# Optimization experiments

Hardware: AMD Instinct MI355X
Metric: run time of the kernel (lower is better)

Reference implementation:

```python
import jax, jax.numpy as jnp
import numpy as np

B, NX, NY = 4, 128, 128
DIM, DH, HEADS, LATENT, DOUT = 128, 64, 8, 64, 128
KM = 3
KD = DH * KM          # per-head low-rank-kernel dim (192)
SCALING = 1.0         # kernel_multiplier<=4 and softmax=False -> scaling_factor
ROT_SCALE = 64.0      # 1/min_freq of continuous RotaryEmbedding (min_freq=1/64)
EPS = 1e-5


def layer_norm(x, g, b):
    m = x.mean(-1, keepdims=True)
    v = jnp.var(x, axis=-1, keepdims=True)
    return (x - m) * jax.lax.rsqrt(v + EPS) * g + b


def pooling_reducer(x, Win, g, b, W1, b1, W2, b2):
    # x: [b, n, m, c] -> mean over axis 2 -> PreNorm(MLP with gated GELU) -> [b, n, latent]
    h = (x @ Win).mean(axis=2)
    h = layer_norm(h, g, b)
    h = h @ W1 + b1
    c = h.shape[-1] // 2
    h = jax.nn.gelu(h[..., :c], approximate=False) * h[..., c:]
    return h @ W2 + b2


def rotary(t, pos):
    # t: [b,h,n,d], pos: [n] continuous coordinates
    d = t.shape[-1]
    inv_freq = 1.0 / (10000.0 ** (jnp.arange(0, d, 2, dtype=jnp.float32) / d))
    f = (pos * ROT_SCALE)[:, None] * inv_freq          # [n, d//2]
    f = jnp.concatenate([f, f], axis=-1)               # [n, d]
    cos, sin = jnp.cos(f), jnp.sin(f)
    x1, x2 = jnp.split(t, 2, axis=-1)
    rot = jnp.concatenate([-x2, x1], axis=-1)          # rotate_half (half-split variant)
    return t * cos + rot * sin


def low_rank_kernel(u, pos, Wqk):
    # u: [b, n, latent] -> kernel K: [b, h, n, n]
    b, n, _ = u.shape
    qk = u @ Wqk                                       # [b, n, 2*h*KD]
    q, k = jnp.split(qk, 2, axis=-1)
    q = q.reshape(b, n, HEADS, KD).transpose(0, 2, 1, 3)
    k = k.reshape(b, n, HEADS, KD).transpose(0, 2, 1, 3)
    q = rotary(q, pos)
    k = rotary(k, pos)
    return jnp.einsum('bhid,bhjd->bhij', q, k) * SCALING


def setup_inputs():
    key = jax.random.key(0)
    ks = jax.random.split(key, 16)
    s = 0.02
    def rn(k, shape):
        return jax.random.normal(k, shape, dtype=jnp.float32) * s
    return {
        'u': jax.random.normal(ks[0], (B, NX, NY, DIM), dtype=jnp.float32),
        'pos_x': jnp.sort(jax.random.uniform(ks[1], (NX,), dtype=jnp.float32)),
        'pos_y': jnp.sort(jax.random.uniform(ks[2], (NY,), dtype=jnp.float32)),
        'ln_g': jnp.ones((DIM,), jnp.float32),
        'ln_b': jnp.zeros((DIM,), jnp.float32),
        'Wv': rn(ks[3], (DIM, HEADS * DH)),
        'Win': rn(ks[4], (DIM, DIM)),
        'px_Win': rn(ks[5], (DIM, DIM)),
        'px_g': jnp.ones((DIM,), jnp.float32),
        'px_b': jnp.zeros((DIM,), jnp.float32),
        'px_W1': rn(ks[6], (DIM, 2 * DIM)),
        'px_b1': jnp.zeros((2 * DIM,), jnp.float32),
        'px_W2': rn(ks[7], (DIM, LATENT)),
        'px_b2': jnp.zeros((LATENT,), jnp.float32),
        'py_Win': rn(ks[8], (DIM, DIM)),
        'py_g': jnp.ones((DIM,), jnp.float32),
        'py_b': jnp.zeros((DIM,), jnp.float32),
        'py_W1': rn(ks[9], (DIM, 2 * DIM)),
        'py_b1': jnp.zeros((2 * DIM,), jnp.float32),
        'py_W2': rn(ks[10], (DIM, LATENT)),
        'py_b2': jnp.zeros((LATENT,), jnp.float32),
        'Wqk_x': rn(ks[11], (LATENT, 2 * HEADS * KD)),
        'Wqk_y': rn(ks[12], (LATENT, 2 * HEADS * KD)),
        'Wo1': rn(ks[13], (HEADS * DH, DOUT)),
        'Wo2': rn(ks[14], (DOUT, DOUT)),
    }


def reference(u, pos_x, pos_y, ln_g, ln_b, Wv, Win,
              px_Win, px_g, px_b, px_W1, px_b1, px_W2, px_b2,
              py_Win, py_g, py_b, py_W1, py_b1, py_W2, py_b2,
              Wqk_x, Wqk_y, Wo1, Wo2):
    un = layer_norm(u, ln_g, ln_b)                      # [b,nx,ny,dim]
    v = un @ Wv                                         # [b,nx,ny,h*dh]
    ui = un @ Win
    ux = pooling_reducer(ui, px_Win, px_g, px_b, px_W1, px_b1, px_W2, px_b2)                       # [b,nx,L]
    uy = pooling_reducer(ui.transpose(0, 2, 1, 3), py_Win, py_g, py_b, py_W1, py_b1, py_W2, py_b2)  # [b,ny,L]
    kx = low_rank_kernel(ux, pos_x, Wqk_x)              # [b,h,nx,nx]
    ky = low_rank_kernel(uy, pos_y, Wqk_y)              # [b,h,ny,ny]
    b, nx, ny, _ = u.shape
    vphi = v.reshape(b, nx, ny, HEADS, DH).transpose(0, 3, 1, 2, 4)   # b h i l c
    t = jnp.einsum('bhij,bhjmc->bhimc', kx, vphi)       # attend along x axis
    t = jnp.einsum('bhlm,bhimc->bhilc', ky, t)          # attend along y axis
    t = t.transpose(0, 2, 3, 1, 4).reshape(b, nx, ny, HEADS * DH)
    # InstanceNorm2d applied to a channels-LAST tensor (as in the original repo):
    # torch treats dim1 (nx) as channels, normalizing over (ny, h*dh) per (b, nx), no affine.
    m = t.mean(axis=(2, 3), keepdims=True)
    var = t.var(axis=(2, 3), keepdims=True)
    t = (t - m) * jax.lax.rsqrt(var + EPS)
    h = jax.nn.gelu(t @ Wo1, approximate=False)
    return h @ Wo2
```

## Files before the change

kernel.cpp:

```cpp
#include <hip/hip_runtime.h>
#include <math.h>

#define ROWS 65536
#define KDD 192

typedef __attribute__((ext_vector_type(8))) short bfrag;
typedef __attribute__((ext_vector_type(4))) float facc;

__device__ inline unsigned short bf16r(float x) {
  union { float f; unsigned u; } v; v.f = x;
  unsigned r = v.u + 0x7fffu + ((v.u >> 16) & 1u);
  return (unsigned short)(r >> 16);
}
__device__ inline float bf2f(unsigned short h) {
  union { unsigned u; float f; } v; v.u = ((unsigned)h) << 16; return v.f;
}
__device__ inline float gelu_f(float x) {
  return x * 0.5f * (1.f + erff(x * 0.70710678f));
}
__device__ __forceinline__ void gload16(const void* g, void* l) {
  __builtin_amdgcn_global_load_lds((const __attribute__((address_space(1))) unsigned int*)g,
                                   (__attribute__((address_space(3))) unsigned int*)l,
                                   16, 0, 0);
}

__global__ __launch_bounds__(256) void k_ln(const float* __restrict__ x,
                                            const float* __restrict__ g,
                                            const float* __restrict__ bb,
                                            unsigned short* __restrict__ y) {
  int t = threadIdx.x;
  int w = t >> 6, lane = t & 63;
  size_t row = (size_t)blockIdx.x * 4 + w;
  float2 v = *(const float2*)(x + row * 128 + lane * 2);
  float s = v.x + v.y, s2 = v.x * v.x + v.y * v.y;
#pragma unroll
  for (int off = 1; off < 64; off <<= 1) {
    s += __shfl_xor(s, off, 64);
    s2 += __shfl_xor(s2, off, 64);
  }
  float mean = s * (1.f / 128.f);
  float var = s2 * (1.f / 128.f) - mean * mean;
  float r = rsqrtf(var + 1e-5f);
  float2 gg = *(const float2*)(g + lane * 2);
  float2 bv = *(const float2*)(bb + lane * 2);
  unsigned h0 = bf16r((v.x - mean) * r * gg.x + bv.x);
  unsigned h1 = bf16r((v.y - mean) * r * gg.y + bv.y);
  *(unsigned*)(y + row * 128 + lane * 2) = h0 | (h1 << 16);
}

__global__ __launch_bounds__(128) void k_means(const unsigned short* __restrict__ un,
                                               float* __restrict__ mx, float* __restrict__ my) {
  int blk = blockIdx.x;
  int c = threadIdx.x;
  if (blk < 512) {
    const unsigned short* p = un + (size_t)blk * 16384 + c;
    float s = 0;
    for (int j = 0; j < 128; j++) s += bf2f(p[(size_t)j * 128]);
    mx[(size_t)blk * 128 + c] = s * (1.f / 128.f);
  } else {
    int bj = blk - 512;
    int b = bj >> 7, j = bj & 127;
    const unsigned short* p = un + (size_t)b * 2097152 + (size_t)j * 128 + c;
    float s = 0;
    for (int i = 0; i < 128; i++) s += bf2f(p[(size_t)i * 16384]);
    my[(size_t)bj * 128 + c] = s * (1.f / 128.f);
  }
}

__global__ __launch_bounds__(256) void k_wprep(const float* __restrict__ Wv,
                                               const float* __restrict__ Wo1,
                                               const float* __restrict__ Wo2,
                                               unsigned short* __restrict__ WvT,
                                               unsigned short* __restrict__ Wo1T,
                                               unsigned short* __restrict__ Wo2T,
                                               float* __restrict__ scol) {
  int blk = blockIdx.x, t = threadIdx.x;
  if (blk < 256) {
    int idx = blk * 256 + t;
    int c = idx >> 7, r = idx & 127;
    WvT[(size_t)c * 128 + r] = bf16r(Wv[(size_t)r * 512 + c]);
  } else if (blk < 512) {
    int idx = (blk - 256) * 256 + t;
    int n = idx >> 9, k = idx & 511;
    Wo1T[(size_t)n * 512 + k] = bf16r(Wo1[(size_t)k * 128 + n]);
  } else if (blk < 576) {
    int idx = (blk - 512) * 256 + t;
    int n = idx >> 7, k = idx & 127;
    Wo2T[n * 128 + k] = bf16r(Wo2[k * 128 + n]);
  } else {
    if (t < 128) {
      float a = 0;
      for (int k = 0; k < 512; k++) a += bf2f(bf16r(Wo1[k * 128 + t]));
      scol[t] = a;
    }
  }
}

__global__ __launch_bounds__(256) void k_gemmz(const float* __restrict__ A0,
                                               const float* __restrict__ B0,
                                               float* __restrict__ C0,
                                               const float* __restrict__ A1,
                                               const float* __restrict__ B1,
                                               float* __restrict__ C1,
                                               int K, int lda, int ldb, int ldc) {
  const float* A = blockIdx.z ? A1 : A0;
  const float* Bm = blockIdx.z ? B1 : B0;
  float* C = blockIdx.z ? C1 : C0;
  __shared__ float As[16][64];
  __shared__ float Bs[16][64];
  int tid = threadIdx.x;
  int n0 = blockIdx.x * 64, m0 = blockIdx.y * 64;
  int tx = tid & 15, ty = tid >> 4;
  float acc[4][4] = {};
  int la_m = tid >> 2, la_k = (tid & 3) * 4;
  int lb_k = tid >> 4, lb_n = (tid & 15) * 4;
  for (int k0 = 0; k0 < K; k0 += 16) {
    float4 a4 = *(const float4*)(A + (size_t)(m0 + la_m) * lda + k0 + la_k);
    As[la_k + 0][la_m] = a4.x; As[la_k + 1][la_m] = a4.y;
    As[la_k + 2][la_m] = a4.z; As[la_k + 3][la_m] = a4.w;
    float4 b4 = *(const float4*)(Bm + (size_t)(k0 + lb_k) * ldb + n0 + lb_n);
    *(float4*)&Bs[lb_k][lb_n] = b4;
    __syncthreads();
#pragma unroll
    for (int kk = 0; kk < 16; kk++) {
      float4 av = *(const float4*)&As[kk][ty * 4];
      float4 bv = *(const float4*)&Bs[kk][tx * 4];
      float a[4] = {av.x, av.y, av.z, av.w};
      float b[4] = {bv.x, bv.y, bv.z, bv.w};
#pragma unroll
      for (int i = 0; i < 4; i++)
#pragma unroll
        for (int j = 0; j < 4; j++) acc[i][j] += a[i] * b[j];
    }
    __syncthreads();
  }
#pragma unroll
  for (int i = 0; i < 4; i++) {
    float4 o;
    o.x = acc[i][0]; o.y = acc[i][1]; o.z = acc[i][2]; o.w = acc[i][3];
    *(float4*)(C + (size_t)(m0 + ty * 4 + i) * ldc + n0 + tx * 4) = o;
  }
}

__global__ __launch_bounds__(128) void k_pool2(const float* __restrict__ in0, const float* __restrict__ in1,
                                               const float* __restrict__ Wc0, const float* __restrict__ Wc1,
                                               const float* __restrict__ g0, const float* __restrict__ g1,
                                               const float* __restrict__ bb0, const float* __restrict__ bb1,
                                               const float* __restrict__ W10, const float* __restrict__ W11,
                                               const float* __restrict__ b10, const float* __restrict__ b11,
                                               const float* __restrict__ W20, const float* __restrict__ W21,
                                               const float* __restrict__ b20, const float* __restrict__ b21,
                                               float* __restrict__ o0, float* __restrict__ o1) {
  int sel = blockIdx.y;
  const float* in = sel ? in1 : in0;  const float* Wc = sel ? Wc1 : Wc0;
  const float* g = sel ? g1 : g0;     const float* bb = sel ? bb1 : bb0;
  const float* W1 = sel ? W11 : W10;  const float* b1 = sel ? b11 : b10;
  const float* W2 = sel ? W21 : W20;  const float* b2 = sel ? b21 : b20;
  float* out = sel ? o1 : o0;
  int row = blockIdx.x;
  int t = threadIdx.x;
  __shared__ float xin[128], h1[128], h3[128];
  __shared__ float ps[2], ps2[2];
  xin[t] = in[(size_t)row * 128 + t];
  __syncthreads();
  float a = 0;
  for (int k = 0; k < 128; k++) a += xin[k] * Wc[k * 128 + t];
  float s = a, s2 = a * a;
  for (int off = 32; off > 0; off >>= 1) {
    s += __shfl_down(s, off, 64);
    s2 += __shfl_down(s2, off, 64);
  }
  if ((t & 63) == 0) { ps[t >> 6] = s; ps2[t >> 6] = s2; }
  __syncthreads();
  float S = ps[0] + ps[1], S2 = ps2[0] + ps2[1];
  float mean = S * (1.f / 128.f);
  float var = S2 * (1.f / 128.f) - mean * mean;
  float r = rsqrtf(var + 1e-5f);
  h1[t] = (a - mean) * r * g[t] + bb[t];
  __syncthreads();
  float u1 = b1[t], u2 = b1[t + 128];
  for (int k = 0; k < 128; k++) {
    float hv = h1[k];
    u1 += hv * W1[k * 256 + t];
    u2 += hv * W1[k * 256 + t + 128];
  }
  h3[t] = gelu_f(u1) * u2;
  __syncthreads();
  if (t < 64) {
    float o = b2[t];
    for (int k = 0; k < 128; k++) o += h3[k] * W2[k * 64 + t];
    out[(size_t)row * 64 + t] = o;
  }
}

__global__ __launch_bounds__(192) void k_rot2(const float* __restrict__ qk0, const float* __restrict__ qk1,
                                              const float* __restrict__ pos0, const float* __restrict__ pos1,
                                              float* __restrict__ qr0, float* __restrict__ qr1,
                                              float* __restrict__ kr0, float* __restrict__ kr1) {
  int sel = blockIdx.y;
  const float* qk = sel ? qk1 : qk0;
  const float* pos = sel ? pos1 : pos0;
  float* qr = sel ? qr1 : qr0;
  float* kr = sel ? kr1 : kr0;
  int bn = blockIdx.x;
  int b = bn >> 7, n = bn & 127;
  int d = threadIdx.x;
  int fi = d % 96;
  float inv = expf(-logf(10000.f) * ((float)fi / 96.f));
  float f = pos[n] * 64.f * inv;
  float cs = cosf(f), sn = sinf(f);
  int partner = d < 96 ? d + 96 : d - 96;
  float sgn = d < 96 ? -1.f : 1.f;
  for (int h = 0; h < 8; h++) {
    float q = qk[(size_t)bn * 3072 + h * 192 + d];
    float qp = qk[(size_t)bn * 3072 + h * 192 + partner];
    float kx = qk[(size_t)bn * 3072 + 1536 + h * 192 + d];
    float kp = qk[(size_t)bn * 3072 + 1536 + h * 192 + partner];
    size_t o = ((size_t)(b * 8 + h) * 128 + n) * 192 + d;
    qr[o] = q * cs + sgn * qp * sn;
    kr[o] = kx * cs + sgn * kp * sn;
  }
}

__global__ __launch_bounds__(512) void k_qkt2(const float* __restrict__ Q0, const float* __restrict__ K0,
                                              unsigned short* __restrict__ C0,
                                              const float* __restrict__ Q1, const float* __restrict__ K1,
                                              unsigned short* __restrict__ C1) {
  int z = blockIdx.z;
  int bh = z & 31;
  const float* Qb = (z < 32 ? Q0 : Q1) + (size_t)bh * 128 * KDD;
  const float* Kb = (z < 32 ? K0 : K1) + (size_t)bh * 128 * KDD;
  unsigned short* Cb = (z < 32 ? C0 : C1) + (size_t)bh * 128 * 128;
  __shared__ float As[16][64];
  __shared__ float Bs[16][64];
  int tid = threadIdx.x;
  int i0 = blockIdx.y * 64, j0 = blockIdx.x * 64;
  int tx = tid & 15, ty = tid >> 4;
  float acc[2][4] = {};
  int l_m = tid >> 3, l_k = (tid & 7) * 2;
  for (int k0 = 0; k0 < KDD; k0 += 16) {
    float2 a2 = *(const float2*)(Qb + (size_t)(i0 + l_m) * KDD + k0 + l_k);
    As[l_k + 0][l_m] = a2.x; As[l_k + 1][l_m] = a2.y;
    float2 b2 = *(const float2*)(Kb + (size_t)(j0 + l_m) * KDD + k0 + l_k);
    Bs[l_k + 0][l_m] = b2.x; Bs[l_k + 1][l_m] = b2.y;
    __syncthreads();
#pragma unroll
    for (int kk = 0; kk < 16; kk++) {
      float2 av = *(const float2*)&As[kk][ty * 2];
      float4 bv = *(const float4*)&Bs[kk][tx * 4];
      float a[2] = {av.x, av.y};
      float b[4] = {bv.x, bv.y, bv.z, bv.w};
#pragma unroll
      for (int i = 0; i < 2; i++)
#pragma unroll
        for (int j = 0; j < 4; j++) acc[i][j] += a[i] * b[j];
    }
    __syncthreads();
  }
#pragma unroll
  for (int i = 0; i < 2; i++) {
    unsigned h0 = bf16r(acc[i][0]), h1 = bf16r(acc[i][1]);
    unsigned h2 = bf16r(acc[i][2]), h3 = bf16r(acc[i][3]);
    uint2 pk;
    pk.x = h0 | (h1 << 16);
    pk.y = h2 | (h3 << 16);
    *(uint2*)(Cb + (size_t)(i0 + ty * 2 + i) * 128 + j0 + tx * 4) = pk;
  }
}


__global__ __launch_bounds__(256) void k_vt(const unsigned short* __restrict__ WvT,
                                            const unsigned short* __restrict__ un,
                                            unsigned short* __restrict__ vT) {
  int nt = blockIdx.x;
  __shared__ __align__(16) unsigned short Bs[16384];
  int tid = threadIdx.x;
  int w = tid >> 6, lane = tid & 63, quad = lane >> 4, l16 = lane & 15;
  int wr = w >> 1, wc = w & 1;
  {
    const unsigned short* sbp = un + (size_t)nt * 16384;
#pragma unroll
    for (int q = 0; q < 8; q++) {
      int rbase = w * 32 + q * 4;
      int r = rbase + quad;
      gload16(sbp + (size_t)r * 128 + ((l16 ^ (r & 15)) << 3), &Bs[rbase * 128]);
    }
  }
  __syncthreads();
  facc zf = {0.f, 0.f, 0.f, 0.f};
#pragma unroll
  for (int mt = 0; mt < 4; mt++) {
    const unsigned short* ap = WvT + (size_t)mt * 128 * 128;
    facc acc[4][4];
#pragma unroll
    for (int lt = 0; lt < 4; lt++)
#pragma unroll
      for (int xt = 0; xt < 4; xt++) acc[lt][xt] = zf;
#pragma unroll
    for (int k0 = 0; k0 < 4; k0++) {
      int chunk = ((k0 * 4 + quad) ^ l16) << 3;
      bfrag bv[4], av[4];
#pragma unroll
      for (int lt = 0; lt < 4; lt++)
        bv[lt] = *(const bfrag*)&Bs[((wc * 4 + lt) * 16 + l16) * 128 + chunk];
#pragma unroll
      for (int xt = 0; xt < 4; xt++)
        av[xt] = *(const bfrag*)(ap + (size_t)((wr * 4 + xt) * 16 + l16) * 128 + k0 * 32 + quad * 8);
      __builtin_amdgcn_s_setprio(1);
#pragma unroll
      for (int lt = 0; lt < 4; lt++)
#pragma unroll
        for (int xt = 0; xt < 4; xt++)
          acc[lt][xt] = __builtin_amdgcn_mfma_f32_16x16x32_bf16(bv[lt], av[xt], acc[lt][xt], 0, 0, 0);
      __builtin_amdgcn_s_setprio(0);
    }
#pragma unroll
    for (int xt = 0; xt < 4; xt++) {
      int hc = mt * 128 + (wr * 4 + xt) * 16 + l16;
      unsigned short* dst = vT + (size_t)hc * 65536 + nt * 128 + quad * 4;
#pragma unroll
      for (int lt = 0; lt < 4; lt++) {
        facc a = acc[lt][xt];
        uint2 p;
        p.x = (unsigned)bf16r(a[0]) | ((unsigned)bf16r(a[1]) << 16);
        p.y = (unsigned)bf16r(a[2]) | ((unsigned)bf16r(a[3]) << 16);
        *(uint2*)(dst + (wc * 4 + lt) * 16) = p;
      }
    }
  }
}

__global__ __launch_bounds__(256, 2) void k_fuse12(const unsigned short* __restrict__ kxall,
                                                   const unsigned short* __restrict__ kyall,
                                                   const unsigned short* __restrict__ vT,
                                                   unsigned short* __restrict__ ttp,
                                                   float* __restrict__ sb,
                                                   float* __restrict__ s2b) {
  int blk = blockIdx.x;
  int bh = blk >> 4, strip = blk & 15;
  int b = bh >> 3, h = bh & 7;
  __shared__ __align__(16) unsigned short Ky[16384];
  __shared__ __align__(16) unsigned short Vs[16384];
  int tid = threadIdx.x;
  int w = tid >> 6, lane = tid & 63, quad = lane >> 4, l16 = lane & 15;
  int wr = w >> 1, wc = w & 1;

  {
    const unsigned short* kb = kyall + (size_t)bh * 16384;
#pragma unroll
    for (int q = 0; q < 8; q++) {
      int rbase = w * 32 + q * 4;
      int r = rbase + quad;
      gload16(kb + (size_t)r * 128 + ((l16 ^ (r & 15)) << 3), &Ky[rbase * 128]);
    }
  }
  bfrag axf[4][4];
  {
    const unsigned short* xb = kxall + (size_t)bh * 16384;
#pragma unroll
    for (int it = 0; it < 4; it++) {
      int i = (wr * 4 + it) * 16 + l16;
#pragma unroll
      for (int k0 = 0; k0 < 4; k0++)
        axf[it][k0] = *(const bfrag*)(xb + (size_t)i * 128 + k0 * 32 + quad * 8);
    }
  }

  float s[4] = {0.f, 0.f, 0.f, 0.f}, s2[4] = {0.f, 0.f, 0.f, 0.f};
  facc zf = {0.f, 0.f, 0.f, 0.f};

  for (int cc = 0; cc < 4; cc++) {
    int c = strip * 4 + cc;
    if (cc) __syncthreads();
    {
      const unsigned short* vb = vT + (size_t)(h * 64 + c) * 65536 + (size_t)b * 16384;
#pragma unroll
      for (int q = 0; q < 8; q++) {
        int rbase = w * 32 + q * 4;
        int r = rbase + quad;
        gload16(vb + (size_t)r * 128 + ((l16 ^ (r & 15)) << 3), &Vs[rbase * 128]);
      }
    }
    __syncthreads();

    facc a1[4][4];
#pragma unroll
    for (int xt = 0; xt < 4; xt++)
#pragma unroll
      for (int lt = 0; lt < 4; lt++) a1[xt][lt] = zf;
#pragma unroll
    for (int k0 = 0; k0 < 4; k0++) {
      int chunk = ((k0 * 4 + quad) ^ l16) << 3;
      bfrag av[4], bv[4];
#pragma unroll
      for (int xt = 0; xt < 4; xt++)
        av[xt] = *(const bfrag*)&Vs[((wr * 4 + xt) * 16 + l16) * 128 + chunk];
#pragma unroll
      for (int lt = 0; lt < 4; lt++)
        bv[lt] = *(const bfrag*)&Ky[((wc * 4 + lt) * 16 + l16) * 128 + chunk];
      __builtin_amdgcn_s_setprio(1);
#pragma unroll
      for (int xt = 0; xt < 4; xt++)
#pragma unroll
        for (int lt = 0; lt < 4; lt++)
          a1[xt][lt] = __builtin_amdgcn_mfma_f32_16x16x32_bf16(av[xt], bv[lt], a1[xt][lt], 0, 0, 0);
      __builtin_amdgcn_s_setprio(0);
    }
    __syncthreads();
#pragma unroll
    for (int xt = 0; xt < 4; xt++) {
      int xc = (wr * 4 + xt) * 2 + (quad >> 1);
      int xo = (quad & 1) * 4;
#pragma unroll
      for (int lt = 0; lt < 4; lt++) {
        int l = (wc * 4 + lt) * 16 + l16;
        unsigned p0 = (unsigned)bf16r(a1[xt][lt][0]) | ((unsigned)bf16r(a1[xt][lt][1]) << 16);
        unsigned p1 = (unsigned)bf16r(a1[xt][lt][2]) | ((unsigned)bf16r(a1[xt][lt][3]) << 16);
        uint2 p; p.x = p0; p.y = p1;
        *(uint2*)&Vs[l * 128 + ((xc ^ (l & 15)) << 3) + xo] = p;
      }
    }
    __syncthreads();

    facc a2[4][4];
#pragma unroll
    for (int st = 0; st < 4; st++)
#pragma unroll
      for (int it = 0; it < 4; it++) a2[st][it] = zf;
#pragma unroll
    for (int k0 = 0; k0 < 4; k0++) {
      int chunk = ((k0 * 4 + quad) ^ l16) << 3;
      bfrag sv[4];
#pragma unroll
      for (int st = 0; st < 4; st++)
        sv[st] = *(const bfrag*)&Vs[((wc * 4 + st) * 16 + l16) * 128 + chunk];
      __builtin_amdgcn_s_setprio(1);
#pragma unroll
      for (int st = 0; st < 4; st++)
#pragma unroll
        for (int it = 0; it < 4; it++)
          a2[st][it] = __builtin_amdgcn_mfma_f32_16x16x32_bf16(sv[st], axf[it][k0], a2[st][it], 0, 0, 0);
      __builtin_amdgcn_s_setprio(0);
    }
    {
      unsigned short* dst = ttp + ((size_t)(bh * 64 + c) << 14);
#pragma unroll
      for (int st = 0; st < 4; st++) {
        int l0 = (wc * 4 + st) * 16 + quad * 4;
#pragma unroll
        for (int it = 0; it < 4; it++) {
          int i = (wr * 4 + it) * 16 + l16;
          float f0 = a2[st][it][0], f1 = a2[st][it][1];
          float f2 = a2[st][it][2], f3 = a2[st][it][3];
          unsigned p0 = (unsigned)bf16r(f0) | ((unsigned)bf16r(f1) << 16);
          unsigned p1 = (unsigned)bf16r(f2) | ((unsigned)bf16r(f3) << 16);
          uint2 p; p.x = p0; p.y = p1;
          *(uint2*)(dst + (size_t)i * 128 + l0) = p;
          s[it] += (f0 + f1) + (f2 + f3);
          s2[it] += f0 * f0 + f1 * f1 + f2 * f2 + f3 * f3;
        }
      }
    }
  }
#pragma unroll
  for (int it = 0; it < 4; it++) {
    float v = s[it], v2 = s2[it];
    v += __shfl_xor(v, 16, 64);  v += __shfl_xor(v, 32, 64);
    v2 += __shfl_xor(v2, 16, 64); v2 += __shfl_xor(v2, 32, 64);
    if (quad == 0) {
      int i = (wr * 4 + it) * 16 + l16;
      atomicAdd(&sb[b * 128 + i], v);
      atomicAdd(&s2b[b * 128 + i], v2);
    }
  }
}

__global__ __launch_bounds__(256) void k_tail2(const unsigned short* __restrict__ ttp,
                                               const unsigned short* __restrict__ Wo1T,
                                               const unsigned short* __restrict__ Wo2T,
                                               float* __restrict__ out,
                                               const float* __restrict__ sb,
                                               const float* __restrict__ s2b,
                                               const float* __restrict__ sc) {
  int blk = blockIdx.x;
  int b = blk >> 7, i = blk & 127;
  __shared__ __align__(16) unsigned short As[16384];
  __shared__ __align__(16) unsigned short Bs[16384];
  int tid = threadIdx.x;
  int w = tid >> 6, lane = tid & 63, quad = lane >> 4, l16 = lane & 15;
  facc zf = {0.f, 0.f, 0.f, 0.f};
  facc a1[2][8];
#pragma unroll
  for (int a = 0; a < 2; a++)
#pragma unroll
    for (int bq = 0; bq < 8; bq++) a1[a][bq] = zf;
  for (int kc = 0; kc < 4; kc++) {
    if (kc) __syncthreads();
    {
      int r = tid >> 1, half = tid & 1;
      int hc = kc * 128 + r;
      const unsigned short* src = ttp + (((size_t)(b * 8 + (hc >> 6)) * 64 + (hc & 63)) * 128 + i) * 128 + half * 64;
#pragma unroll
      for (int q = 0; q < 8; q++) {
        uint4 v = *(const uint4*)(src + q * 8);
        unsigned short* pv = (unsigned short*)&v;
#pragma unroll
        for (int e = 0; e < 8; e++) {
          int l = half * 64 + q * 8 + e;
          As[l * 128 + (((r >> 3) ^ (l & 15)) << 3) + (r & 7)] = pv[e];
        }
      }
      const unsigned short* sB = Wo1T + (size_t)r * 512 + kc * 128 + half * 64;
#pragma unroll
      for (int q = 0; q < 8; q++) {
        int c8 = half * 8 + q;
        *(uint4*)&Bs[r * 128 + ((c8 ^ (r & 15)) << 3)] = *(const uint4*)(sB + q * 8);
      }
    }
    __syncthreads();
#pragma unroll
    for (int k0 = 0; k0 < 4; k0++) {
      bfrag av[2];
#pragma unroll
      for (int it = 0; it < 2; it++) {
        int row = (w + it * 4) * 16 + l16;
        av[it] = *(const bfrag*)&As[row * 128 + (((k0 * 4 + quad) ^ l16) << 3)];
      }
#pragma unroll
      for (int nt = 0; nt < 8; nt++) {
        int row = nt * 16 + l16;
        bfrag bv = *(const bfrag*)&Bs[row * 128 + (((k0 * 4 + quad) ^ l16) << 3)];
        a1[0][nt] = __builtin_amdgcn_mfma_f32_16x16x32_bf16(av[0], bv, a1[0][nt], 0, 0, 0);
        a1[1][nt] = __builtin_amdgcn_mfma_f32_16x16x32_bf16(av[1], bv, a1[1][nt], 0, 0, 0);
      }
    }
  }
  float S = sb[b * 128 + i], S2 = s2b[b * 128 + i];
  float mean = S * (1.f / 65536.f);
  float var = S2 * (1.f / 65536.f) - mean * mean;
  float rs = rsqrtf(var + 1e-5f);
  __syncthreads();
#pragma unroll
  for (int it = 0; it < 2; it++)
#pragma unroll
    for (int nt = 0; nt < 8; nt++) {
      int n1 = nt * 16 + l16;
      float scn = sc[n1];
#pragma unroll
      for (int rr = 0; rr < 4; rr++) {
        int l = (w + it * 4) * 16 + quad * 4 + rr;
        float val = (a1[it][nt][rr] - mean * scn) * rs;
        As[l * 128 + (((n1 >> 3) ^ (l & 15)) << 3) + (n1 & 7)] = bf16r(gelu_f(val));
      }
    }
  {
    int r = tid >> 1, half = tid & 1;
    const unsigned short* sB = Wo2T + (size_t)r * 128 + half * 64;
#pragma unroll
    for (int q = 0; q < 8; q++) {
      int c8 = half * 8 + q;
      *(uint4*)&Bs[r * 128 + ((c8 ^ (r & 15)) << 3)] = *(const uint4*)(sB + q * 8);
    }
  }
  __syncthreads();
  facc a2[2][8];
#pragma unroll
  for (int a = 0; a < 2; a++)
#pragma unroll
    for (int bq = 0; bq < 8; bq++) a2[a][bq] = zf;
#pragma unroll
  for (int k0 = 0; k0 < 4; k0++) {
    bfrag av[2];
#pragma unroll
    for (int it = 0; it < 2; it++) {
      int row = (w + it * 4) * 16 + l16;
      av[it] = *(const bfrag*)&As[row * 128 + (((k0 * 4 + quad) ^ l16) << 3)];
    }
#pragma unroll
    for (int nt = 0; nt < 8; nt++) {
      int row = nt * 16 + l16;
      bfrag bv = *(const bfrag*)&Bs[row * 128 + (((k0 * 4 + quad) ^ l16) << 3)];
      a2[0][nt] = __builtin_amdgcn_mfma_f32_16x16x32_bf16(av[0], bv, a2[0][nt], 0, 0, 0);
      a2[1][nt] = __builtin_amdgcn_mfma_f32_16x16x32_bf16(av[1], bv, a2[1][nt], 0, 0, 0);
    }
  }
#pragma unroll
  for (int it = 0; it < 2; it++)
#pragma unroll
    for (int nt = 0; nt < 8; nt++) {
      int n2 = nt * 16 + l16;
#pragma unroll
      for (int rr = 0; rr < 4; rr++) {
        int l = (w + it * 4) * 16 + quad * 4 + rr;
        out[((size_t)(b * 16384 + i * 128 + l)) * 128 + n2] = a2[it][nt][rr];
      }
    }
}

extern "C" void kernel_launch(void* const* d_in, const int* in_sizes, int n_in,
                              void* d_out, int out_size, void* d_ws, size_t ws_size,
                              hipStream_t stream) {
  const float* u = (const float*)d_in[0];
  const float* pos_x = (const float*)d_in[1];
  const float* pos_y = (const float*)d_in[2];
  const float* ln_g = (const float*)d_in[3];
  const float* ln_b = (const float*)d_in[4];
  const float* Wv = (const float*)d_in[5];
  const float* Win = (const float*)d_in[6];
  const float* px_Win = (const float*)d_in[7];
  const float* px_g = (const float*)d_in[8];
  const float* px_b = (const float*)d_in[9];
  const float* px_W1 = (const float*)d_in[10];
  const float* px_b1 = (const float*)d_in[11];
  const float* px_W2 = (const float*)d_in[12];
  const float* px_b2 = (const float*)d_in[13];
  const float* py_Win = (const float*)d_in[14];
  const float* py_g = (const float*)d_in[15];
  const float* py_b = (const float*)d_in[16];
  const float* py_W1 = (const float*)d_in[17];
  const float* py_b1 = (const float*)d_in[18];
  const float* py_W2 = (const float*)d_in[19];
  const float* py_b2 = (const float*)d_in[20];
  const float* Wqk_x = (const float*)d_in[21];
  const float* Wqk_y = (const float*)d_in[22];
  const float* Wo1 = (const float*)d_in[23];
  const float* Wo2 = (const float*)d_in[24];
  float* out = (float*)d_out;

  const size_t NEED = 44868736;
  if (ws_size < NEED * sizeof(float)) return;
  float* ws = (float*)d_ws;
  unsigned short* un_bf = (unsigned short*)ws;
  unsigned short* vT    = (unsigned short*)(ws + 4194304);
  unsigned short* ttp   = (unsigned short*)(ws + 20971520);
  float* small = ws + 37748736;
  float* mun_x = small;
  float* mun_y = small + 65536;
  float* Wcx   = small + 131072;
  float* Wcy   = small + 147456;
  float* ux    = small + 163840;
  float* uy    = small + 196608;
  float* qkx   = small + 229376;
  float* qky   = small + 1802240;
  float* qrx   = small + 3375104;
  float* krx   = small + 4161536;
  float* qry   = small + 4947968;
  float* kry   = small + 5734400;
  unsigned short* kx_bf = (unsigned short*)(small + 6520832);
  unsigned short* ky_bf = (unsigned short*)(small + 6782976);
  unsigned short* WvT   = (unsigned short*)(small + 7045120);
  unsigned short* Wo1T  = (unsigned short*)(small + 7077888);
  unsigned short* Wo2T  = (unsigned short*)(small + 7110656);
  float* sbuf  = small + 7118848;
  float* s2buf = small + 7119360;
  float* scol  = small + 7119872;

  hipMemsetAsync(sbuf, 0, 1024 * sizeof(float), stream);

  k_ln<<<16384, 256, 0, stream>>>(u, ln_g, ln_b, un_bf);
  k_means<<<1024, 128, 0, stream>>>(un_bf, mun_x, mun_y);
  k_wprep<<<577, 256, 0, stream>>>(Wv, Wo1, Wo2, WvT, Wo1T, Wo2T, scol);
  k_gemmz<<<dim3(2, 2, 2), 256, 0, stream>>>(Win, px_Win, Wcx, Win, py_Win, Wcy,
                                             128, 128, 128, 128);
  k_pool2<<<dim3(512, 2), 128, 0, stream>>>(mun_x, mun_y, Wcx, Wcy, px_g, py_g, px_b, py_b,
                                            px_W1, py_W1, px_b1, py_b1, px_W2, py_W2,
                                            px_b2, py_b2, ux, uy);
  k_gemmz<<<dim3(48, 8, 2), 256, 0, stream>>>(ux, Wqk_x, qkx, uy, Wqk_y, qky,
                                              64, 64, 3072, 3072);
  k_rot2<<<dim3(512, 2), 192, 0, stream>>>(qkx, qky, pos_x, pos_y, qrx, qry, krx, kry);
  k_qkt2<<<dim3(2, 2, 64), 512, 0, stream>>>(qrx, krx, kx_bf, qry, kry, ky_bf);

  k_vt<<<512, 256, 0, stream>>>(WvT, un_bf, vT);
  k_fuse12<<<512, 256, 0, stream>>>(kx_bf, ky_bf, vT, ttp, sbuf, s2buf);
  k_tail2<<<512, 256, 0, stream>>>(ttp, Wo1T, Wo2T, out, sbuf, s2buf, scol);
}
```

Before: 317.0 us.

## Merge prep kernels into LayerNorm launch, fuse means and rotary into consumers

Folds the weight-transpose prep, the Win composite GEMM and a new cos/sin table build into the LayerNorm kernel as extra block ranges. The per-axis mean computation moves into the pooling kernel, and rotary embedding is applied on the fly while loading tiles in the QK^T kernel using the precomputed table. This removes four kernel launches and the qr/kr intermediate round trip through memory. In exchange the QK^T loader does more gathers and arithmetic per tile, and the pooling kernel now performs strided reductions itself.

```diff
diff --git a/kernel.cpp b/kernel.cpp
--- a/kernel.cpp
+++ b/kernel.cpp
@@ -1,7 +1,6 @@
 #include <hip/hip_runtime.h>
 #include <math.h>
 
-#define ROWS 65536
 #define KDD 192
 
 typedef __attribute__((ext_vector_type(8))) short bfrag;
@@ -24,75 +23,184 @@
                                    16, 0, 0);
 }
 
-__global__ __launch_bounds__(256) void k_ln(const float* __restrict__ x,
-                                            const float* __restrict__ g,
-                                            const float* __restrict__ bb,
-                                            unsigned short* __restrict__ y) {
+__global__ __launch_bounds__(256) void k_lnw(const float* __restrict__ x,
+                                             const float* __restrict__ g,
+                                             const float* __restrict__ bb,
+                                             unsigned short* __restrict__ y,
+                                             const float* __restrict__ Wv,
+                                             const float* __restrict__ Wo1,
+                                             const float* __restrict__ Wo2,
+                                             unsigned short* __restrict__ WvT,
+                                             unsigned short* __restrict__ Wo1T,
+                                             unsigned short* __restrict__ Wo2T,
+                                             float* __restrict__ scol,
+                                             const float* __restrict__ Win,
+                                             const float* __restrict__ pxW,
+                                             const float* __restrict__ pyW,
+                                             float* __restrict__ Wcx,
+                                             float* __restrict__ Wcy,
+                                             const float* __restrict__ pos_x,
+                                             const float* __restrict__ pos_y,
+                                             float* __restrict__ tabx,
+                                             float* __restrict__ taby) {
+  __shared__ float As[16][64];
+  __shared__ float Bs[16][64];
+  int bid = blockIdx.x, t = threadIdx.x;
+  if (bid < 16384) {
+    int w = t >> 6, lane = t & 63;
+    size_t row = (size_t)bid * 4 + w;
+    float2 v = *(const float2*)(x + row * 128 + lane * 2);
+    float s = v.x + v.y, s2 = v.x * v.x + v.y * v.y;
+#pragma unroll
+    for (int off = 1; off < 64; off <<= 1) {
+      s += __shfl_xor(s, off, 64);
+      s2 += __shfl_xor(s2, off, 64);
+    }
+    float mean = s * (1.f / 128.f);
+    float var = s2 * (1.f / 128.f) - mean * mean;
+    float r = rsqrtf(var + 1e-5f);
+    float2 gg = *(const float2*)(g + lane * 2);
+    float2 bv = *(const float2*)(bb + lane * 2);
+    unsigned h0 = bf16r((v.x - mean) * r * gg.x + bv.x);
+    unsigned h1 = bf16r((v.y - mean) * r * gg.y + bv.y);
+    *(unsigned*)(y + row * 128 + lane * 2) = h0 | (h1 << 16);
+    return;
+  }
+  if (bid < 16961) {
+    int blk = bid - 16384;
+    if (blk < 256) {
+      int idx = blk * 256 + t;
+      int c = idx >> 7, r = idx & 127;
+      WvT[(size_t)c * 128 + r] = bf16r(Wv[(size_t)r * 512 + c]);
+    } else if (blk < 512) {
+      int idx = (blk - 256) * 256 + t;
+      int n = idx >> 9, k = idx & 511;
+      Wo1T[(size_t)n * 512 + k] = bf16r(Wo1[(size_t)k * 128 + n]);
+    } else if (blk < 576) {
+      int idx = (blk - 512) * 256 + t;
+      int n = idx >> 7, k = idx & 127;
+      Wo2T[n * 128 + k] = bf16r(Wo2[k * 128 + n]);
+    } else {
+      if (t < 128) {
+        float a = 0;
+        for (int k = 0; k < 512; k++) a += bf2f(bf16r(Wo1[k * 128 + t]));
+        scol[t] = a;
+      }
+    }
+    return;
+  }
+  if (bid < 16969) {
+    int idx = bid - 16961;
+    int n0 = (idx & 1) * 64, m0 = ((idx >> 1) & 1) * 64;
+    const float* A = Win;
+    const float* Bm = (idx >> 2) ? pyW : pxW;
+    float* C = (idx >> 2) ? Wcy : Wcx;
+    int tx = t & 15, ty = t >> 4;
+    float acc[4][4] = {};
+    int la_m = t >> 2, la_k = (t & 3) * 4;
+    int lb_k = t >> 4, lb_n = (t & 15) * 4;
+    for (int k0 = 0; k0 < 128; k0 += 16) {
+      float4 a4 = *(const float4*)(A + (size_t)(m0 + la_m) * 128 + k0 + la_k);
+      As[la_k + 0][la_m] = a4.x; As[la_k + 1][la_m] = a4.y;
+      As[la_k + 2][la_m] = a4.z; As[la_k + 3][la_m] = a4.w;
+      float4 b4 = *(const float4*)(Bm + (size_t)(k0 + lb_k) * 128 + n0 + lb_n);
+      *(float4*)&Bs[lb_k][lb_n] = b4;
+      __syncthreads();
+#pragma unroll
+      for (int kk = 0; kk < 16; kk++) {
+        float4 av = *(const float4*)&As[kk][ty * 4];
+        float4 bv = *(const float4*)&Bs[kk][tx * 4];
+        float a[4] = {av.x, av.y, av.z, av.w};
+        float b[4] = {bv.x, bv.y, bv.z, bv.w};
+#pragma unroll
+        for (int i = 0; i < 4; i++)
+#pragma unroll
+          for (int j = 0; j < 4; j++) acc[i][j] += a[i] * b[j];
+      }
+      __syncthreads();
+    }
+#pragma unroll
+    for (int i = 0; i < 4; i++) {
+      float4 o;
+      o.x = acc[i][0]; o.y = acc[i][1]; o.z = acc[i][2]; o.w = acc[i][3];
+      *(float4*)(C + (size_t)(m0 + ty * 4 + i) * 128 + n0 + tx * 4) = o;
+    }
+    return;
+  }
+  {
+    int id = (bid - 16969) * 256 + t;
+    int axis = id >= 12288;
+    int rem = axis ? id - 12288 : id;
+    int n = rem / 96, fi = rem - n * 96;
+    const float* pos = axis ? pos_y : pos_x;
+    float inv = expf(-logf(10000.f) * ((float)fi / 96.f));
+    float f = pos[n] * 64.f * inv;
+    float2 cssn;
+    cssn.x = cosf(f);
+    cssn.y = sinf(f);
+    ((float2*)(axis ? taby : tabx))[n * 96 + fi] = cssn;
+  }
+}
+
+__global__ __launch_bounds__(128) void k_pool2(const unsigned short* __restrict__ un,
+                                               const float* __restrict__ Wc0, const float* __restrict__ Wc1,
+                                               const float* __restrict__ g0, const float* __restrict__ g1,
+                                               const float* __restrict__ bb0, const float* __restrict__ bb1,
+                                               const float* __restrict__ W10, const float* __restrict__ W11,
+                                               const float* __restrict__ b10, const float* __restrict__ b11,
+                                               const float* __restrict__ W20, const float* __restrict__ W21,
+                                               const float* __restrict__ b20, const float* __restrict__ b21,
+                                               float* __restrict__ o0, float* __restrict__ o1) {
+  int sel = blockIdx.y;
+  const float* Wc = sel ? Wc1 : Wc0;
+  const float* g = sel ? g1 : g0;     const float* bb = sel ? bb1 : bb0;
+  const float* W1 = sel ? W11 : W10;  const float* b1 = sel ? b11 : b10;
+  const float* W2 = sel ? W21 : W20;  const float* b2 = sel ? b21 : b20;
+  float* out = sel ? o1 : o0;
+  int row = blockIdx.x;
   int t = threadIdx.x;
-  int w = t >> 6, lane = t & 63;
-  size_t row = (size_t)blockIdx.x * 4 + w;
-  float2 v = *(const float2*)(x + row * 128 + lane * 2);
-  float s = v.x + v.y, s2 = v.x * v.x + v.y * v.y;
-#pragma unroll
-  for (int off = 1; off < 64; off <<= 1) {
-    s += __shfl_xor(s, off, 64);
-    s2 += __shfl_xor(s2, off, 64);
-  }
-  float mean = s * (1.f / 128.f);
-  float var = s2 * (1.f / 128.f) - mean * mean;
+  __shared__ float xin[128], h1[128], h3[128];
+  __shared__ float ps[2], ps2[2];
+  {
+    float s0 = 0.f;
+    if (sel == 0) {
+      const unsigned short* p = un + (size_t)row * 16384 + t;
+      for (int j = 0; j < 128; j++) s0 += bf2f(p[(size_t)j * 128]);
+    } else {
+      int b = row >> 7, j = row & 127;
+      const unsigned short* p = un + (size_t)b * 2097152 + (size_t)j * 128 + t;
+      for (int i = 0; i < 128; i++) s0 += bf2f(p[(size_t)i * 16384]);
+    }
+    xin[t] = s0 * (1.f / 128.f);
+  }
+  __syncthreads();
+  float a = 0;
+  for (int k = 0; k < 128; k++) a += xin[k] * Wc[k * 128 + t];
+  float s = a, s2 = a * a;
+  for (int off = 32; off > 0; off >>= 1) {
+    s += __shfl_down(s, off, 64);
+    s2 += __shfl_down(s2, off, 64);
+  }
+  if ((t & 63) == 0) { ps[t >> 6] = s; ps2[t >> 6] = s2; }
+  __syncthreads();
+  float S = ps[0] + ps[1], S2 = ps2[0] + ps2[1];
+  float mean = S * (1.f / 128.f);
+  float var = S2 * (1.f / 128.f) - mean * mean;
   float r = rsqrtf(var + 1e-5f);
-  float2 gg = *(const float2*)(g + lane * 2);
-  float2 bv = *(const float2*)(bb + lane * 2);
-  unsigned h0 = bf16r((v.x - mean) * r * gg.x + bv.x);
-  unsigned h1 = bf16r((v.y - mean) * r * gg.y + bv.y);
-  *(unsigned*)(y + row * 128 + lane * 2) = h0 | (h1 << 16);
-}
-
-__global__ __launch_bounds__(128) void k_means(const unsigned short* __restrict__ un,
-                                               float* __restrict__ mx, float* __restrict__ my) {
-  int blk = blockIdx.x;
-  int c = threadIdx.x;
-  if (blk < 512) {
-    const unsigned short* p = un + (size_t)blk * 16384 + c;
-    float s = 0;
-    for (int j = 0; j < 128; j++) s += bf2f(p[(size_t)j * 128]);
-    mx[(size_t)blk * 128 + c] = s * (1.f / 128.f);
-  } else {
-    int bj = blk - 512;
-    int b = bj >> 7, j = bj & 127;
-    const unsigned short* p = un + (size_t)b * 2097152 + (size_t)j * 128 + c;
-    float s = 0;
-    for (int i = 0; i < 128; i++) s += bf2f(p[(size_t)i * 16384]);
-    my[(size_t)bj * 128 + c] = s * (1.f / 128.f);
-  }
-}
-
-__global__ __launch_bounds__(256) void k_wprep(const float* __restrict__ Wv,
-                                               const float* __restrict__ Wo1,
-                                               const float* __restrict__ Wo2,
-                                               unsigned short* __restrict__ WvT,
-                                               unsigned short* __restrict__ Wo1T,
-                                               unsigned short* __restrict__ Wo2T,
-                                               float* __restrict__ scol) {
-  int blk = blockIdx.x, t = threadIdx.x;
-  if (blk < 256) {
-    int idx = blk * 256 + t;
-    int c = idx >> 7, r = idx & 127;
-    WvT[(size_t)c * 128 + r] = bf16r(Wv[(size_t)r * 512 + c]);
-  } else if (blk < 512) {
-    int idx = (blk - 256) * 256 + t;
-    int n = idx >> 9, k = idx & 511;
-    Wo1T[(size_t)n * 512 + k] = bf16r(Wo1[(size_t)k * 128 + n]);
-  } else if (blk < 576) {
-    int idx = (blk - 512) * 256 + t;
-    int n = idx >> 7, k = idx & 127;
-    Wo2T[n * 128 + k] = bf16r(Wo2[k * 128 + n]);
-  } else {
-    if (t < 128) {
-      float a = 0;
-      for (int k = 0; k < 512; k++) a += bf2f(bf16r(Wo1[k * 128 + t]));
-      scol[t] = a;
-    }
+  h1[t] = (a - mean) * r * g[t] + bb[t];
+  __syncthreads();
+  float u1 = b1[t], u2 = b1[t + 128];
+  for (int k = 0; k < 128; k++) {
+    float hv = h1[k];
+    u1 += hv * W1[k * 256 + t];
+    u2 += hv * W1[k * 256 + t + 128];
+  }
+  h3[t] = gelu_f(u1) * u2;
+  __syncthreads();
+  if (t < 64) {
+    float o = b2[t];
+    for (int k = 0; k < 128; k++) o += h3[k] * W2[k * 64 + t];
+    out[(size_t)row * 64 + t] = o;
   }
 }
 
@@ -142,95 +250,16 @@
   }
 }
 
-__global__ __launch_bounds__(128) void k_pool2(const float* __restrict__ in0, const float* __restrict__ in1,
-                                               const float* __restrict__ Wc0, const float* __restrict__ Wc1,
-                                               const float* __restrict__ g0, const float* __restrict__ g1,
-                                               const float* __restrict__ bb0, const float* __restrict__ bb1,
-                                               const float* __restrict__ W10, const float* __restrict__ W11,
-                                               const float* __restrict__ b10, const float* __restrict__ b11,
-                                               const float* __restrict__ W20, const float* __restrict__ W21,
-                                               const float* __restrict__ b20, const float* __restrict__ b21,
-                                               float* __restrict__ o0, float* __restrict__ o1) {
-  int sel = blockIdx.y;
-  const float* in = sel ? in1 : in0;  const float* Wc = sel ? Wc1 : Wc0;
-  const float* g = sel ? g1 : g0;     const float* bb = sel ? bb1 : bb0;
-  const float* W1 = sel ? W11 : W10;  const float* b1 = sel ? b11 : b10;
-  const float* W2 = sel ? W21 : W20;  const float* b2 = sel ? b21 : b20;
-  float* out = sel ? o1 : o0;
-  int row = blockIdx.x;
-  int t = threadIdx.x;
-  __shared__ float xin[128], h1[128], h3[128];
-  __shared__ float ps[2], ps2[2];
-  xin[t] = in[(size_t)row * 128 + t];
-  __syncthreads();
-  float a = 0;
-  for (int k = 0; k < 128; k++) a += xin[k] * Wc[k * 128 + t];
-  float s = a, s2 = a * a;
-  for (int off = 32; off > 0; off >>= 1) {
-    s += __shfl_down(s, off, 64);
-    s2 += __shfl_down(s2, off, 64);
-  }
-  if ((t & 63) == 0) { ps[t >> 6] = s; ps2[t >> 6] = s2; }
-  __syncthreads();
-  float S = ps[0] + ps[1], S2 = ps2[0] + ps2[1];
-  float mean = S * (1.f / 128.f);
-  float var = S2 * (1.f / 128.f) - mean * mean;
-  float r = rsqrtf(var + 1e-5f);
-  h1[t] = (a - mean) * r * g[t] + bb[t];
-  __syncthreads();
-  float u1 = b1[t], u2 = b1[t + 128];
-  for (int k = 0; k < 128; k++) {
-    float hv = h1[k];
-    u1 += hv * W1[k * 256 + t];
-    u2 += hv * W1[k * 256 + t + 128];
-  }
-  h3[t] = gelu_f(u1) * u2;
-  __syncthreads();
-  if (t < 64) {
-    float o = b2[t];
-    for (int k = 0; k < 128; k++) o += h3[k] * W2[k * 64 + t];
-    out[(size_t)row * 64 + t] = o;
-  }
-}
-
-__global__ __launch_bounds__(192) void k_rot2(const float* __restrict__ qk0, const float* __restrict__ qk1,
-                                              const float* __restrict__ pos0, const float* __restrict__ pos1,
-                                              float* __restrict__ qr0, float* __restrict__ qr1,
-                                              float* __restrict__ kr0, float* __restrict__ kr1) {
-  int sel = blockIdx.y;
-  const float* qk = sel ? qk1 : qk0;
-  const float* pos = sel ? pos1 : pos0;
-  float* qr = sel ? qr1 : qr0;
-  float* kr = sel ? kr1 : kr0;
-  int bn = blockIdx.x;
-  int b = bn >> 7, n = bn & 127;
-  int d = threadIdx.x;
-  int fi = d % 96;
-  float inv = expf(-logf(10000.f) * ((float)fi / 96.f));
-  float f = pos[n] * 64.f * inv;
-  float cs = cosf(f), sn = sinf(f);
-  int partner = d < 96 ? d + 96 : d - 96;
-  float sgn = d < 96 ? -1.f : 1.f;
-  for (int h = 0; h < 8; h++) {
-    float q = qk[(size_t)bn * 3072 + h * 192 + d];
-    float qp = qk[(size_t)bn * 3072 + h * 192 + partner];
-    float kx = qk[(size_t)bn * 3072 + 1536 + h * 192 + d];
-    float kp = qk[(size_t)bn * 3072 + 1536 + h * 192 + partner];
-    size_t o = ((size_t)(b * 8 + h) * 128 + n) * 192 + d;
-    qr[o] = q * cs + sgn * qp * sn;
-    kr[o] = kx * cs + sgn * kp * sn;
-  }
-}
-
-__global__ __launch_bounds__(512) void k_qkt2(const float* __restrict__ Q0, const float* __restrict__ K0,
+__global__ __launch_bounds__(512) void k_qkt2(const float* __restrict__ qk0, const float* __restrict__ qk1,
+                                              const float* __restrict__ tab0, const float* __restrict__ tab1,
                                               unsigned short* __restrict__ C0,
-                                              const float* __restrict__ Q1, const float* __restrict__ K1,
                                               unsigned short* __restrict__ C1) {
   int z = blockIdx.z;
   int bh = z & 31;
-  const float* Qb = (z < 32 ? Q0 : Q1) + (size_t)bh * 128 * KDD;
-  const float* Kb = (z < 32 ? K0 : K1) + (size_t)bh * 128 * KDD;
-  unsigned short* Cb = (z < 32 ? C0 : C1) + (size_t)bh * 128 * 128;
+  int b = bh >> 3, h = bh & 7;
+  const float* qk = (z < 32) ? qk0 : qk1;
+  const float* tab = (z < 32) ? tab0 : tab1;
+  unsigned short* Cb = ((z < 32) ? C0 : C1) + (size_t)bh * 16384;
   __shared__ float As[16][64];
   __shared__ float Bs[16][64];
   int tid = threadIdx.x;
@@ -239,21 +268,41 @@
   float acc[2][4] = {};
   int l_m = tid >> 3, l_k = (tid & 7) * 2;
   for (int k0 = 0; k0 < KDD; k0 += 16) {
-    float2 a2 = *(const float2*)(Qb + (size_t)(i0 + l_m) * KDD + k0 + l_k);
-    As[l_k + 0][l_m] = a2.x; As[l_k + 1][l_m] = a2.y;
-    float2 b2 = *(const float2*)(Kb + (size_t)(j0 + l_m) * KDD + k0 + l_k);
-    Bs[l_k + 0][l_m] = b2.x; Bs[l_k + 1][l_m] = b2.y;
+    int d = k0 + l_k;
+    int fi = d < 96 ? d : d - 96;
+    float sgn = d < 96 ? -1.f : 1.f;
+    int prt = d < 96 ? d + 96 : d - 96;
+    {
+      int n = i0 + l_m;
+      const float* src = qk + (size_t)(b * 128 + n) * 3072 + h * 192;
+      float2 qd = *(const float2*)(src + d);
+      float2 qp = *(const float2*)(src + prt);
+      float2 t0 = *(const float2*)(tab + (size_t)(n * 96 + fi) * 2);
+      float2 t1 = *(const float2*)(tab + (size_t)(n * 96 + fi + 1) * 2);
+      As[l_k + 0][l_m] = qd.x * t0.x + sgn * qp.x * t0.y;
+      As[l_k + 1][l_m] = qd.y * t1.x + sgn * qp.y * t1.y;
+    }
+    {
+      int n = j0 + l_m;
+      const float* src = qk + (size_t)(b * 128 + n) * 3072 + 1536 + h * 192;
+      float2 qd = *(const float2*)(src + d);
+      float2 qp = *(const float2*)(src + prt);
+      float2 t0 = *(const float2*)(tab + (size_t)(n * 96 + fi) * 2);
+      float2 t1 = *(const float2*)(tab + (size_t)(n * 96 + fi + 1) * 2);
+      Bs[l_k + 0][l_m] = qd.x * t0.x + sgn * qp.x * t0.y;
+      Bs[l_k + 1][l_m] = qd.y * t1.x + sgn * qp.y * t1.y;
+    }
     __syncthreads();
 #pragma unroll
     for (int kk = 0; kk < 16; kk++) {
       float2 av = *(const float2*)&As[kk][ty * 2];
       float4 bv = *(const float4*)&Bs[kk][tx * 4];
       float a[2] = {av.x, av.y};
-      float b[4] = {bv.x, bv.y, bv.z, bv.w};
+      float b2[4] = {bv.x, bv.y, bv.z, bv.w};
 #pragma unroll
       for (int i = 0; i < 2; i++)
 #pragma unroll
-        for (int j = 0; j < 4; j++) acc[i][j] += a[i] * b[j];
+        for (int j = 0; j < 4; j++) acc[i][j] += a[i] * b2[j];
     }
     __syncthreads();
   }
@@ -634,18 +683,14 @@
   unsigned short* vT    = (unsigned short*)(ws + 4194304);
   unsigned short* ttp   = (unsigned short*)(ws + 20971520);
   float* small = ws + 37748736;
-  float* mun_x = small;
-  float* mun_y = small + 65536;
   float* Wcx   = small + 131072;
   float* Wcy   = small + 147456;
   float* ux    = small + 163840;
   float* uy    = small + 196608;
   float* qkx   = small + 229376;
   float* qky   = small + 1802240;
-  float* qrx   = small + 3375104;
-  float* krx   = small + 4161536;
-  float* qry   = small + 4947968;
-  float* kry   = small + 5734400;
+  float* tabx  = small + 3375104;
+  float* taby  = small + 3399680;
   unsigned short* kx_bf = (unsigned short*)(small + 6520832);
   unsigned short* ky_bf = (unsigned short*)(small + 6782976);
   unsigned short* WvT   = (unsigned short*)(small + 7045120);
@@ -657,18 +702,16 @@
 
   hipMemsetAsync(sbuf, 0, 1024 * sizeof(float), stream);
 
-  k_ln<<<16384, 256, 0, stream>>>(u, ln_g, ln_b, un_bf);
-  k_means<<<1024, 128, 0, stream>>>(un_bf, mun_x, mun_y);
-  k_wprep<<<577, 256, 0, stream>>>(Wv, Wo1, Wo2, WvT, Wo1T, Wo2T, scol);
-  k_gemmz<<<dim3(2, 2, 2), 256, 0, stream>>>(Win, px_Win, Wcx, Win, py_Win, Wcy,
-                                             128, 128, 128, 128);
-  k_pool2<<<dim3(512, 2), 128, 0, stream>>>(mun_x, mun_y, Wcx, Wcy, px_g, py_g, px_b, py_b,
+  k_lnw<<<17065, 256, 0, stream>>>(u, ln_g, ln_b, un_bf, Wv, Wo1, Wo2,
+                                   WvT, Wo1T, Wo2T, scol,
+                                   Win, px_Win, py_Win, Wcx, Wcy,
+                                   pos_x, pos_y, tabx, taby);
+  k_pool2<<<dim3(512, 2), 128, 0, stream>>>(un_bf, Wcx, Wcy, px_g, py_g, px_b, py_b,
                                             px_W1, py_W1, px_b1, py_b1, px_W2, py_W2,
                                             px_b2, py_b2, ux, uy);
   k_gemmz<<<dim3(48, 8, 2), 256, 0, stream>>>(ux, Wqk_x, qkx, uy, Wqk_y, qky,
                                               64, 64, 3072, 3072);
-  k_rot2<<<dim3(512, 2), 192, 0, stream>>>(qkx, qky, pos_x, pos_y, qrx, qry, krx, kry);
-  k_qkt2<<<dim3(2, 2, 64), 512, 0, stream>>>(qrx, krx, kx_bf, qry, kry, ky_bf);
+  k_qkt2<<<dim3(2, 2, 64), 512, 0, stream>>>(qkx, qky, tabx, taby, kx_bf, ky_bf);
 
   k_vt<<<512, 256, 0, stream>>>(WvT, un_bf, vT);
   k_fuse12<<<512, 256, 0, stream>>>(kx_bf, ky_bf, vT, ttp, sbuf, s2buf);
```

Result: faster. 296.3 us (-6.5%).
